# Performance work log

Measured on AMD Instinct MI355X. Metric: run time of the kernel, lower is better.

The kernel has to match this reference:

```python
import math
import jax, jax.numpy as jnp
import numpy as np

DIM = 512
STYLE_DIM = 512
WS = 8
RES = 64
HEADS = 16
SHIFT = WS // 2
B = 8
EPS = 1e-5


def _rel_pos_index(ws):
    # Faithful replica of the (non-standard) index construction in the source.
    coords = np.stack(np.meshgrid(np.arange(ws), np.arange(ws), indexing='ij')).reshape(2, -1)
    rc = (coords[:, :, None] - coords[:, None, :]).transpose(1, 2, 0).astype(np.int64)
    rc[:, :, 0] += ws - 1
    rc[:, :, 1] += ws - 1
    rc[:, :, 0] += 2 * ws - 1
    return jnp.asarray(rc.sum(-1))  # (ws*ws, ws*ws)


def _attn_mask2(res, ws):
    shift = ws // 2
    m = np.zeros((res, res), dtype=np.float32)
    cnt = 0
    for hs in [slice(0, -ws), slice(-ws, -shift), slice(-shift, None)]:
        for wsl in [slice(0, -ws), slice(-ws, -shift), slice(-shift, None)]:
            m[hs, wsl] = cnt
            cnt += 1
    mw = m.reshape(res // ws, ws, res // ws, ws).transpose(0, 2, 1, 3).reshape(-1, ws * ws)
    am = mw[:, None, :] - mw[:, :, None]  # (nW, N, N)
    return jnp.asarray(np.where(am != 0, -100.0, 0.0).astype(np.float32))


_RPI = _rel_pos_index(WS)
_MASK2 = _attn_mask2(RES, WS)


def _win_part(x, ws):
    Bc, H, W, C = x.shape
    x = x.reshape(Bc, H // ws, ws, W // ws, ws, C).transpose(0, 1, 3, 2, 4, 5)
    return x.reshape(-1, ws * ws, C)


def _win_rev(x, ws, H, W):
    nH, nW = H // ws, W // ws
    C = x.shape[-1]
    x = x.reshape(-1, nH, nW, ws, ws, C).transpose(0, 1, 3, 2, 4, 5)
    return x.reshape(-1, H, W, C)


def _adain(x, style, w, b):
    # x: (B, N, C); InstanceNorm1d over the token dim N per channel (biased var, no affine).
    scale = 1.0 / math.sqrt(w.shape[1])
    s = style @ (w * scale).T + b  # (B, 2C)
    C = x.shape[-1]
    gamma, beta = s[:, :C], s[:, C:]
    mean = x.mean(axis=1, keepdims=True)
    var = x.var(axis=1, keepdims=True)
    xn = (x - mean) / jnp.sqrt(var + EPS)
    return gamma[:, None, :] * xn + beta[:, None, :]


def _window_attn(q, k, v, ws, heads, rpb, rpi, mask):
    # q/k/v: (B, H, W, C)
    C = q.shape[-1]
    hd = C // heads
    qk_scale = hd ** -0.5
    qw = _win_part(q, ws)  # (Bw, N, C)
    kw = _win_part(k, ws)
    vw = _win_part(v, ws)
    Bw, N, _ = qw.shape
    qw = qw.reshape(Bw, N, heads, hd).transpose(0, 2, 1, 3)
    kw = kw.reshape(Bw, N, heads, hd).transpose(0, 2, 1, 3)
    vw = vw.reshape(Bw, N, heads, hd).transpose(0, 2, 1, 3)
    attn = jnp.einsum('bhnd,bhmd->bhnm', qw, kw) * qk_scale
    bias = rpb[rpi.reshape(-1)].reshape(N, N, heads).transpose(2, 0, 1)  # (h, N, N)
    attn = attn + bias[None]
    if mask is not None:
        nW = mask.shape[0]
        attn = attn.reshape(Bw // nW, nW, heads, N, N) + mask[None, :, None]
        attn = attn.reshape(Bw, heads, N, N)
    attn = jax.nn.softmax(attn, axis=-1)
    out = jnp.einsum('bhnm,bhmd->bhnd', attn, vw)
    return out.transpose(0, 2, 1, 3).reshape(Bw, N, C)


def _forward(x, style, ada1_w, ada1_b, qkv_w, qkv_b, rpb1, rpb2,
             proj_w, proj_b, ada2_w, ada2_b, mlp_w1, mlp_b1, mlp_w2, mlp_b2):
    H = W = RES
    Bc, N, C = x.shape
    shortcut = x
    xn = _adain(x, style, ada1_w, ada1_b)
    qkv = xn @ qkv_w.T + qkv_b  # (B, N, 3C)
    qkv = qkv.reshape(Bc, N, 3, C).transpose(2, 0, 1, 3).reshape(3, Bc, H, W, C)
    qkv1 = qkv[..., : C // 2]
    qkv2 = qkv[..., C // 2:]
    qkv2 = jnp.roll(qkv2, shift=(-SHIFT, -SHIFT), axis=(2, 3))
    x1 = _window_attn(qkv1[0], qkv1[1], qkv1[2], WS, HEADS // 2, rpb1, _RPI, None)
    x2 = _window_attn(qkv2[0], qkv2[1], qkv2[2], WS, HEADS // 2, rpb2, _RPI, _MASK2)
    x1 = _win_rev(x1, WS, H, W)
    x2 = _win_rev(x2, WS, H, W)
    x2 = jnp.roll(x2, shift=(SHIFT, SHIFT), axis=(1, 2))
    out = jnp.concatenate([x1, x2], axis=-1).reshape(Bc, N, C)
    out = out @ proj_w.T + proj_b
    out = shortcut + out
    xn2 = _adain(out, style, ada2_w, ada2_b)
    h = xn2 @ mlp_w1.T + mlp_b1
    h = jax.nn.gelu(h, approximate=False)  # erf-based gelu matches source
    h = h @ mlp_w2.T + mlp_b2
    return out + h


def setup_inputs() -> dict:
    key = jax.random.key(0)
    ks = jax.random.split(key, 16)
    rn = lambda k, shp, s: jax.random.normal(k, shp, dtype=jnp.float32) * s
    return {
        'x': rn(ks[0], (B, RES * RES, DIM), 1.0),
        'style': rn(ks[1], (B, STYLE_DIM), 1.0),
        'ada1_w': rn(ks[2], (2 * DIM, STYLE_DIM), 1.0),
        'ada1_b': rn(ks[3], (2 * DIM,), 0.02),
        'qkv_w': rn(ks[4], (3 * DIM, DIM), 0.02),
        'qkv_b': rn(ks[5], (3 * DIM,), 0.02),
        'rpb1': rn(ks[6], ((2 * WS - 1) ** 2, HEADS // 2), 0.02),
        'rpb2': rn(ks[7], ((2 * WS - 1) ** 2, HEADS // 2), 0.02),
        'proj_w': rn(ks[8], (DIM, DIM), 0.02),
        'proj_b': rn(ks[9], (DIM,), 0.02),
        'ada2_w': rn(ks[10], (2 * DIM, STYLE_DIM), 1.0),
        'ada2_b': rn(ks[11], (2 * DIM,), 0.02),
        'mlp_w1': rn(ks[12], (4 * DIM, DIM), 0.02),
        'mlp_b1': rn(ks[13], (4 * DIM,), 0.02),
        'mlp_w2': rn(ks[14], (DIM, 4 * DIM), 0.02),
        'mlp_b2': rn(ks[15], (DIM,), 0.02),
    }


def reference(x, style, ada1_w, ada1_b, qkv_w, qkv_b, rpb1, rpb2,
              proj_w, proj_b, ada2_w, ada2_b, mlp_w1, mlp_b1, mlp_w2, mlp_b2):
    return _forward(x, style, ada1_w, ada1_b, qkv_w, qkv_b, rpb1, rpb2,
                    proj_w, proj_b, ada2_w, ada2_b, mlp_w1, mlp_b1, mlp_w2, mlp_b2)
```

## Files before the change

kernel.cpp:

```cpp
#include <hip/hip_runtime.h>
#include <math.h>

typedef __attribute__((ext_vector_type(8))) short short8;
typedef __attribute__((ext_vector_type(4))) float f32x4;
typedef unsigned short ushort_t;
typedef unsigned long long ull_t;

__device__ __forceinline__ float bf2f(ushort_t u) {
    return __uint_as_float(((unsigned int)u) << 16);
}
__device__ __forceinline__ ushort_t f2bf(float f) {
    unsigned int u = __float_as_uint(f);
    unsigned int r = u + 0x7fffu + ((u >> 16) & 1u);
    return (ushort_t)(r >> 16);
}
__device__ __forceinline__ unsigned cvt_pk_bf16(float lo, float hi) {
    unsigned r;
    asm volatile("v_cvt_pk_bf16_f32 %0, %1, %2" : "=v"(r) : "v"(lo), "v"(hi));
    return r;
}

__device__ __forceinline__ void async_cp16(const void* g, void* l) {
    __builtin_amdgcn_global_load_lds((const __attribute__((address_space(1))) void*)g,
                                     (__attribute__((address_space(3))) void*)l, 16, 0, 0);
}

__device__ __forceinline__ float fast_gelu(float v) {
    float u2 = 2.0f * v * (0.7978845608028654f + 0.0356774081f * v * v);
    float e = __expf(u2);
    float r = 1.0f / (e + 1.0f);
    return v - v * r;
}

__global__ __launch_bounds__(256) void conv_zero(
        const float* __restrict__ qkv_w, ushort_t* __restrict__ qkv_wb,
        const float* __restrict__ proj_w, ushort_t* __restrict__ proj_wb,
        const float* __restrict__ w1, ushort_t* __restrict__ w1b,
        const float* __restrict__ w2, ushort_t* __restrict__ w2b,
        float* __restrict__ psum2, float* __restrict__ psq2,
        const float* __restrict__ rpb1, const float* __restrict__ rpb2,
        float* __restrict__ tbl0, float* __restrict__ tbl1) {
    int i = blockIdx.x * 256 + threadIdx.x;
    if (i < 786432) {
        qkv_wb[i] = f2bf(qkv_w[i]);
    } else if (i < 1048576) {
        int j = i - 786432; proj_wb[j] = f2bf(proj_w[j]);
    } else if (i < 2097152) {
        int j = i - 1048576; w1b[j] = f2bf(w1[j]);
    } else if (i < 3145728) {
        int j = i - 2097152; w2b[j] = f2bf(w2[j]);
    } else if (i < 3153920) {
        int j = i - 3145728;
        psum2[j] = 0.f; psq2[j] = 0.f;
    } else {
        int t = i - 3153920;
        if (t < 32768) {
            int h = t >> 12, ij = t & 4095;
            int qi = ij >> 6, kj = ij & 63;
            int idx = ((qi >> 3) - (kj >> 3)) + ((qi & 7) - (kj & 7)) + 29;
            tbl0[t] = rpb1[idx * 8 + h];
        } else {
            int u = t - 32768;
            int ij = u & 4095;
            int cls = (u >> 12) & 3;
            int h = u >> 14;
            int qi = ij >> 6, kj = ij & 63;
            int idx = ((qi >> 3) - (kj >> 3)) + ((qi & 7) - (kj & 7)) + 29;
            float v = rpb2[idx * 8 + h];
            int gh_i = (cls & 2) ? (((qi >> 3) < 4) ? 1 : 2) : 0;
            int gw_i = (cls & 1) ? (((qi & 7) < 4) ? 1 : 2) : 0;
            int gh_j = (cls & 2) ? (((kj >> 3) < 4) ? 1 : 2) : 0;
            int gw_j = (cls & 1) ? (((kj & 7) < 4) ? 1 : 2) : 0;
            if (gh_i * 3 + gw_i != gh_j * 3 + gw_j) v -= 100.f;
            tbl1[u] = v;
        }
    }
}

__global__ __launch_bounds__(256) void style_kernel(const float* __restrict__ style,
        const float* __restrict__ w1, const float* __restrict__ b1,
        const float* __restrict__ w2, const float* __restrict__ b2,
        float* __restrict__ s1, float* __restrict__ s2) {
    int t = blockIdx.x * 256 + threadIdx.x;
    int which = t >> 13;
    int idx = t & 8191;
    int b = idx >> 10, j = idx & 1023;
    const float* w = which ? w2 : w1;
    const float* bb = which ? b2 : b1;
    const float* st = style + b * 512;
    const float* wr = w + (size_t)j * 512;
    float acc = 0.f;
    for (int k = 0; k < 512; ++k) acc += st[k] * wr[k];
    float v = acc * 0.04419417382415922f + bb[j];
    (which ? s2 : s1)[idx] = v;
}

__global__ __launch_bounds__(512) void stats_part(const float* __restrict__ x,
        float* __restrict__ psum, float* __restrict__ psq) {
    int b = blockIdx.x >> 5;
    int ch = blockIdx.x & 31;
    int c = threadIdx.x;
    const float* p = x + ((size_t)b * 4096 + (size_t)ch * 128) * 512 + c;
    float s = 0.f, q = 0.f;
    for (int t = 0; t < 128; ++t) {
        float v = p[(size_t)t * 512];
        s += v; q += v * v;
    }
    psum[(size_t)blockIdx.x * 512 + c] = s;
    psq [(size_t)blockIdx.x * 512 + c] = q;
}

__global__ __launch_bounds__(256) void stats_fin(const float* __restrict__ psum,
        const float* __restrict__ psq, float* __restrict__ mean, float* __restrict__ rstd) {
    int i = blockIdx.x * 256 + threadIdx.x;
    int b = i >> 9, c = i & 511;
    float s = 0.f, q = 0.f;
    for (int ch = 0; ch < 32; ++ch) {
        s += psum[(size_t)(b * 32 + ch) * 512 + c];
        q += psq [(size_t)(b * 32 + ch) * 512 + c];
    }
    float m = s * (1.f / 4096.f);
    float v = q * (1.f / 4096.f) - m * m;
    mean[i] = m;
    rstd[i] = rsqrtf(v + 1e-5f);
}

__global__ __launch_bounds__(256) void stats_fin2(const float* __restrict__ psum2,
        const float* __restrict__ psq2, float* __restrict__ mean, float* __restrict__ rstd) {
    int i = blockIdx.x * 256 + threadIdx.x;
    float m = psum2[i] * (1.f / 4096.f);
    float v = psq2[i] * (1.f / 4096.f) - m * m;
    mean[i] = m;
    rstd[i] = rsqrtf(v + 1e-5f);
}

__global__ __launch_bounds__(256) void adain_kernel(const float* __restrict__ x,
        const float* __restrict__ s, const float* __restrict__ mean,
        const float* __restrict__ rstd, ushort_t* __restrict__ xn) {
    size_t i4 = (size_t)blockIdx.x * 256 + threadIdx.x;
    size_t e = i4 * 4;
    int b = (int)(e >> 21);
    int c = (int)(e & 511);
    float4 xv = *(const float4*)(x + e);
    float vals[4] = {xv.x, xv.y, xv.z, xv.w};
    ushort_t o[4];
#pragma unroll
    for (int j = 0; j < 4; ++j) {
        int cc = c + j;
        float g  = s[b * 1024 + cc];
        float be = s[b * 1024 + 512 + cc];
        float mn = mean[b * 512 + cc];
        float rs = rstd[b * 512 + cc];
        o[j] = f2bf(g * (vals[j] - mn) * rs + be);
    }
    ull_t packed = (ull_t)o[0] |
        ((ull_t)o[1] << 16) | ((ull_t)o[2] << 32) | ((ull_t)o[3] << 48);
    *(ull_t*)(xn + e) = packed;
}

template<int EPI>
__global__ __launch_bounds__(512, 2) void gemm256(
        const ushort_t* __restrict__ A, const ushort_t* __restrict__ Bw,
        const float* __restrict__ bias, const float* __restrict__ resid,
        float* __restrict__ outf, ushort_t* __restrict__ outh,
        float* __restrict__ psum2, float* __restrict__ psq2,
        int N, int K, int gridN, int ntiles, int lnt) {
    __shared__ ushort_t lds[65536];
    const int tid  = threadIdx.x;
    const int lane = tid & 63;
    const int wave = tid >> 6;
    const int wm = wave >> 2, wn = wave & 3;
    const int lm = lane & 15;
    const int kg = lane >> 4;
    const int nt = 1 << lnt;
    const int tpb = ntiles >> 8;

    const int orig = blockIdx.x;
    const int wgid = (orig & 7) * 32 + (orig >> 3);

    unsigned int lo0 = lm * 128 + ((kg * 16) ^ ((lm & 7) << 4));
    unsigned int lo1 = lo0 ^ 64;
    unsigned int vA0 = wm * 16384 + lo0;
    unsigned int vA1 = wm * 16384 + lo1;
    unsigned int vB0 = 65536 + (wn >> 1) * 16384 + (wn & 1) * 8192 + lo0;
    unsigned int vB1 = 65536 + (wn >> 1) * 16384 + (wn & 1) * 8192 + lo1;
    const char* ldsc = (const char*)lds;

    int off[2][2];
#pragma unroll
    for (int rnd = 0; rnd < 2; ++rnd) {
        int chunk = tid + rnd * 512;
        int row = chunk >> 3;
        int g = chunk & 7;
        int gsw = g ^ (row & 7);
#pragma unroll
        for (int h = 0; h < 2; ++h)
            off[h][rnd] = (h * 128 + row) * K + gsw * 8;
    }

    f32x4 acc[8][4];
#pragma unroll
    for (int m = 0; m < 8; ++m)
#pragma unroll
        for (int n = 0; n < 4; ++n)
#pragma unroll
            for (int r = 0; r < 4; ++r) acc[m][n][r] = 0.f;

    auto stage = [&](const ushort_t* __restrict__ mat, long bcur, long bnxt,
                     int dslot, int h, int tt, int isB) {
        long mb = (tt < nt) ? bcur : bnxt;
        int kt = tt & (nt - 1);
        const ushort_t* base = mat + mb + (kt << 6);
        ushort_t* dst = (ushort_t*)lds + isB * 32768 + dslot * 16384 + h * 8192 + tid * 8;
#pragma unroll
        for (int rnd = 0; rnd < 2; ++rnd)
            async_cp16(base + off[h][rnd], dst + rnd * 4096);
    };

    int tcur = wgid;
    int bm = tcur / gridN, bn = tcur - bm * gridN;
    long Am = (long)bm * 256 * K;
    long Bn = (long)bn * 256 * K;

    stage(A,  Am, Am, 0, 0, 0, 0); stage(A,  Am, Am, 0, 1, 0, 0);
    stage(Bw, Bn, Bn, 0, 0, 0, 1); stage(Bw, Bn, Bn, 0, 1, 0, 1);
    stage(Bw, Bn, Bn, 1, 0, 1, 1); stage(Bw, Bn, Bn, 1, 1, 1, 1);
    asm volatile("s_waitcnt vmcnt(4)" ::: "memory");
    __builtin_amdgcn_sched_barrier(0);
    __builtin_amdgcn_s_barrier();
    asm volatile("" ::: "memory");

    for (int ti = 0; ti < tpb; ++ti) {
        int tnxt = (ti + 1 < tpb) ? tcur + 256 : tcur;
        int bm2 = tnxt / gridN, bn2 = tnxt - bm2 * gridN;
        long Am2 = (long)bm2 * 256 * K;
        long Bn2 = (long)bn2 * 256 * K;

#pragma unroll 2
        for (int t = 0; t < nt; ++t) {
            const int c = t & 1;
            short8 bfr[4][2];
#pragma unroll
            for (int q = 0; q < 4; ++q) {
                short8 af[2][2];
#pragma unroll
                for (int mq = 0; mq < 2; ++mq) {
                    af[mq][0] = *(const short8*)(ldsc + vA0 + (q * 4096 + mq * 2048));
                    af[mq][1] = *(const short8*)(ldsc + vA1 + (q * 4096 + mq * 2048));
                }
                if (q == 0) {
#pragma unroll
                    for (int n = 0; n < 4; ++n) {
                        bfr[n][0] = *(const short8*)(ldsc + vB0 + n * 2048);
                        bfr[n][1] = *(const short8*)(ldsc + vB1 + n * 2048);
                    }
                }
                if      (q == 0) stage(A,  Am, Am2, c ^ 1, 0, t + 1, 0);
                else if (q == 1) stage(A,  Am, Am2, c ^ 1, 1, t + 1, 0);
                else if (q == 2) stage(Bw, Bn, Bn2, c,     0, t + 2, 1);
                else             stage(Bw, Bn, Bn2, c,     1, t + 2, 1);

                __builtin_amdgcn_s_setprio(1);
#pragma unroll
                for (int mq = 0; mq < 2; ++mq)
#pragma unroll
                    for (int n = 0; n < 4; ++n)
#pragma unroll
                        for (int ks = 0; ks < 2; ++ks)
                            acc[q * 2 + mq][n] = __builtin_amdgcn_mfma_f32_16x16x32_bf16(
                                af[mq][ks], bfr[n][ks], acc[q * 2 + mq][n], 0, 0, 0);
                __builtin_amdgcn_s_setprio(0);
                if (q == 3) {
                    asm volatile("s_waitcnt vmcnt(4)" ::: "memory");
                    __builtin_amdgcn_sched_barrier(0);
                }
                __builtin_amdgcn_s_barrier();
                asm volatile("" ::: "memory");
            }
            vA0 ^= 32768u; vA1 ^= 32768u; vB0 ^= 32768u; vB1 ^= 32768u;
        }

        const long tile_m = (long)bm * 256;
        const long tile_n = (long)bn * 256;
        float csum[4], csq[4];
        if (EPI == 1) {
#pragma unroll
            for (int n = 0; n < 4; ++n) { csum[n] = 0.f; csq[n] = 0.f; }
        }
#pragma unroll
        for (int m = 0; m < 8; ++m) {
            long row0 = tile_m + wm * 128 + m * 16 + kg * 4;
#pragma unroll
            for (int n = 0; n < 4; ++n) {
                long col = tile_n + wn * 64 + n * 16 + lm;
                float bb = bias[col];
#pragma unroll
                for (int r = 0; r < 4; ++r) {
                    long o = (row0 + r) * (long)N + col;
                    float v = acc[m][n][r] + bb;
                    if (EPI == 0) {
                        outh[o] = f2bf(v);
                    } else if (EPI == 1) {
                        float w = v + resid[o];
                        outf[o] = w;
                        csum[n] += w; csq[n] += w * w;
                    } else if (EPI == 2) {
                        outh[o] = f2bf(fast_gelu(v));
                    } else {
                        outf[o] += v;
                    }
                    acc[m][n][r] = 0.f;
                }
            }
        }
        if (EPI == 1) {
            int b = (int)(tile_m >> 12);
#pragma unroll
            for (int n = 0; n < 4; ++n) {
                int col = (int)(tile_n + wn * 64 + n * 16 + lm);
                atomicAdd(&psum2[b * 512 + col], csum[n]);
                atomicAdd(&psq2 [b * 512 + col], csq[n]);
            }
        }

        tcur = tnxt; bm = bm2; bn = bn2; Am = Am2; Bn = Bn2;
    }
}

__global__ __launch_bounds__(256) void attn_mfma(const ushort_t* __restrict__ qkv,
        const float* __restrict__ tbl0, const float* __restrict__ tbl1,
        ushort_t* __restrict__ attno) {
    __shared__ ushort_t lds[27648];
    const int tid = threadIdx.x;
    const int lane = tid & 63;
    const int wave = tid >> 6;
    const int job = blockIdx.x * 4 + wave;
    const int branch = job >> 12;
    const int w_idx  = (job >> 3) & 511;
    const int head   = job & 7;
    const int b = w_idx >> 6, win = w_idx & 63;
    const int wh = win >> 3, ww = win & 7;
    const int c0 = branch * 256 + head * 32;
    const int i_lo = lane & 15;
    const int kg = lane >> 4;

    ushort_t* Vt = lds + wave * 6912;
    ushort_t* P  = lds + wave * 6912 + 2304;

    auto tokof = [&](int p) {
        int hh = wh * 8 + (p >> 3), wp = ww * 8 + (p & 7);
        if (branch) { hh = (hh + 4) & 63; wp = (wp + 4) & 63; }
        return b * 4096 + hh * 64 + wp;
    };

    {
        const ushort_t* vp = qkv + (size_t)tokof(lane) * 1536 + 1024 + c0;
        short8 v0 = *(const short8*)(vp);
        short8 v1 = *(const short8*)(vp + 8);
        short8 v2 = *(const short8*)(vp + 16);
        short8 v3 = *(const short8*)(vp + 24);
#pragma unroll
        for (int e = 0; e < 8; ++e) {
            Vt[(e     ) * 72 + lane] = (ushort_t)v0[e];
            Vt[(e +  8) * 72 + lane] = (ushort_t)v1[e];
            Vt[(e + 16) * 72 + lane] = (ushort_t)v2[e];
            Vt[(e + 24) * 72 + lane] = (ushort_t)v3[e];
        }
    }

    short8 kf[4], qf[4];
#pragma unroll
    for (int m = 0; m < 4; ++m) {
        size_t rowb = (size_t)tokof(m * 16 + i_lo) * 1536;
        kf[m] = *(const short8*)(qkv + rowb + 512 + c0 + kg * 8);
        qf[m] = *(const short8*)(qkv + rowb + c0 + kg * 8);
    }

    f32x4 s[4][4];
#pragma unroll
    for (int mj = 0; mj < 4; ++mj)
#pragma unroll
        for (int ni = 0; ni < 4; ++ni)
#pragma unroll
            for (int r = 0; r < 4; ++r) s[mj][ni][r] = 0.f;
#pragma unroll
    for (int mj = 0; mj < 4; ++mj)
#pragma unroll
        for (int ni = 0; ni < 4; ++ni)
            s[mj][ni] = __builtin_amdgcn_mfma_f32_16x16x32_bf16(kf[mj], qf[ni], s[mj][ni], 0, 0, 0);

    const float* tb;
    if (branch == 0) {
        tb = tbl0 + head * 4096;
    } else {
        int cls = ((wh == 7) ? 2 : 0) | ((ww == 7) ? 1 : 0);
        tb = tbl1 + (head * 4 + cls) * 4096;
    }
#pragma unroll
    for (int ni = 0; ni < 4; ++ni) {
        int i = ni * 16 + i_lo;
#pragma unroll
        for (int mj = 0; mj < 4; ++mj) {
            float4 bv = *(const float4*)(tb + i * 64 + mj * 16 + kg * 4);
            s[mj][ni][0] = s[mj][ni][0] * 0.17677669529663687f + bv.x;
            s[mj][ni][1] = s[mj][ni][1] * 0.17677669529663687f + bv.y;
            s[mj][ni][2] = s[mj][ni][2] * 0.17677669529663687f + bv.z;
            s[mj][ni][3] = s[mj][ni][3] * 0.17677669529663687f + bv.w;
        }
    }

    float mx[4], rs[4];
#pragma unroll
    for (int ni = 0; ni < 4; ++ni) {
        float m = -1e30f;
#pragma unroll
        for (int mj = 0; mj < 4; ++mj)
#pragma unroll
            for (int r = 0; r < 4; ++r) m = fmaxf(m, s[mj][ni][r]);
        m = fmaxf(m, __shfl_xor(m, 16));
        m = fmaxf(m, __shfl_xor(m, 32));
        mx[ni] = m;
    }
#pragma unroll
    for (int ni = 0; ni < 4; ++ni) {
        float sum = 0.f;
#pragma unroll
        for (int mj = 0; mj < 4; ++mj)
#pragma unroll
            for (int r = 0; r < 4; ++r) {
                float e = __expf(s[mj][ni][r] - mx[ni]);
                s[mj][ni][r] = e;
                sum += e;
            }
        sum += __shfl_xor(sum, 16);
        sum += __shfl_xor(sum, 32);
        rs[ni] = sum;
    }

#pragma unroll
    for (int ni = 0; ni < 4; ++ni) {
        int i = ni * 16 + i_lo;
#pragma unroll
        for (int mj = 0; mj < 4; ++mj) {
            unsigned w0 = cvt_pk_bf16(s[mj][ni][0], s[mj][ni][1]);
            unsigned w1 = cvt_pk_bf16(s[mj][ni][2], s[mj][ni][3]);
            ull_t w = (ull_t)w0 | ((ull_t)w1 << 32);
            *(ull_t*)&P[i * 72 + mj * 16 + kg * 4] = w;
        }
    }
    asm volatile("s_waitcnt lgkmcnt(0)" ::: "memory");
    __builtin_amdgcn_sched_barrier(0);

    short8 va[2][2];
    short8 pb[4][2];
#pragma unroll
    for (int md = 0; md < 2; ++md)
#pragma unroll
        for (int ks = 0; ks < 2; ++ks)
            va[md][ks] = *(const short8*)&Vt[(md * 16 + i_lo) * 72 + ks * 32 + kg * 8];
#pragma unroll
    for (int ni = 0; ni < 4; ++ni)
#pragma unroll
        for (int ks = 0; ks < 2; ++ks)
            pb[ni][ks] = *(const short8*)&P[(ni * 16 + i_lo) * 72 + ks * 32 + kg * 8];

    f32x4 o[2][4];
#pragma unroll
    for (int md = 0; md < 2; ++md)
#pragma unroll
        for (int ni = 0; ni < 4; ++ni)
#pragma unroll
            for (int r = 0; r < 4; ++r) o[md][ni][r] = 0.f;
#pragma unroll
    for (int md = 0; md < 2; ++md)
#pragma unroll
        for (int ni = 0; ni < 4; ++ni)
#pragma unroll
            for (int ks = 0; ks < 2; ++ks)
                o[md][ni] = __builtin_amdgcn_mfma_f32_16x16x32_bf16(va[md][ks], pb[ni][ks], o[md][ni], 0, 0, 0);

#pragma unroll
    for (int ni = 0; ni < 4; ++ni) {
        float inv = 1.f / rs[ni];
        ushort_t* op = attno + (size_t)tokof(ni * 16 + i_lo) * 512 + c0;
#pragma unroll
        for (int md = 0; md < 2; ++md) {
            ushort_t h0 = f2bf(o[md][ni][0] * inv);
            ushort_t h1 = f2bf(o[md][ni][1] * inv);
            ushort_t h2 = f2bf(o[md][ni][2] * inv);
            ushort_t h3 = f2bf(o[md][ni][3] * inv);
            ull_t w = (ull_t)h0 | ((ull_t)h1 << 16) | ((ull_t)h2 << 32) | ((ull_t)h3 << 48);
            *(ull_t*)(op + md * 16 + kg * 4) = w;
        }
    }
}

extern "C" void kernel_launch(void* const* d_in, const int* in_sizes, int n_in,
                              void* d_out, int out_size, void* d_ws, size_t ws_size,
                              hipStream_t stream) {
    const float* x      = (const float*)d_in[0];
    const float* style  = (const float*)d_in[1];
    const float* ada1_w = (const float*)d_in[2];
    const float* ada1_b = (const float*)d_in[3];
    const float* qkv_w  = (const float*)d_in[4];
    const float* qkv_b  = (const float*)d_in[5];
    const float* rpb1   = (const float*)d_in[6];
    const float* rpb2   = (const float*)d_in[7];
    const float* proj_w = (const float*)d_in[8];
    const float* proj_b = (const float*)d_in[9];
    const float* ada2_w = (const float*)d_in[10];
    const float* ada2_b = (const float*)d_in[11];
    const float* mlp_w1 = (const float*)d_in[12];
    const float* mlp_b1 = (const float*)d_in[13];
    const float* mlp_w2 = (const float*)d_in[14];
    const float* mlp_b2 = (const float*)d_in[15];
    float* outf = (float*)d_out;

    char* W = (char*)d_ws;
    ushort_t* qkvb    = (ushort_t*)(W);
    ushort_t* attno   = (ushort_t*)(W + 100663296);
    ushort_t* hbuf    = (ushort_t*)(W);
    ushort_t* xn      = (ushort_t*)(W + 134217728);
    ushort_t* qkv_wb  = (ushort_t*)(W + 167772160);
    ushort_t* proj_wb = (ushort_t*)(W + 167772160 + 1572864);
    ushort_t* w1b     = (ushort_t*)(W + 167772160 + 2097152);
    ushort_t* w2b     = (ushort_t*)(W + 167772160 + 4194304);
    float* freg  = (float*)(W + 167772160 + 6291456);
    float* s1    = freg;
    float* s2    = freg + 8192;
    float* mean1 = freg + 16384;
    float* rstd1 = freg + 20480;
    float* mean2 = freg + 24576;
    float* rstd2 = freg + 28672;
    float* psum  = freg + 32768;
    float* psq   = freg + 163840;
    float* psum2 = freg + 294912;
    float* psq2  = freg + 303104;
    float* tbl0  = freg + 311296;
    float* tbl1  = freg + 344064;

    conv_zero<<<12960, 256, 0, stream>>>(qkv_w, qkv_wb, proj_w, proj_wb,
                                         mlp_w1, w1b, mlp_w2, w2b, psum2, psq2,
                                         rpb1, rpb2, tbl0, tbl1);

    style_kernel<<<64, 256, 0, stream>>>(style, ada1_w, ada1_b, ada2_w, ada2_b, s1, s2);

    stats_part<<<256, 512, 0, stream>>>(x, psum, psq);
    stats_fin<<<16, 256, 0, stream>>>(psum, psq, mean1, rstd1);
    adain_kernel<<<16384, 256, 0, stream>>>(x, s1, mean1, rstd1, xn);

    gemm256<0><<<256, 512, 0, stream>>>(xn, qkv_wb, qkv_b, nullptr, nullptr, qkvb,
                                        nullptr, nullptr, 1536, 512, 6, 768, 3);

    attn_mfma<<<2048, 256, 0, stream>>>(qkvb, tbl0, tbl1, attno);

    gemm256<1><<<256, 512, 0, stream>>>(attno, proj_wb, proj_b, x, outf, nullptr,
                                        psum2, psq2, 512, 512, 2, 256, 3);

    stats_fin2<<<16, 256, 0, stream>>>(psum2, psq2, mean2, rstd2);
    adain_kernel<<<16384, 256, 0, stream>>>(outf, s2, mean2, rstd2, xn);

    gemm256<2><<<256, 512, 0, stream>>>(xn, w1b, mlp_b1, nullptr, nullptr, hbuf,
                                        nullptr, nullptr, 2048, 512, 8, 1024, 3);
    gemm256<3><<<256, 512, 0, stream>>>(hbuf, w2b, mlp_b2, nullptr, outf, nullptr,
                                        nullptr, nullptr, 512, 2048, 2, 256, 5);
}
```

Baseline: 423.1 us.

## Split style dot products, widen AdaIN vectors, simplify GEMM B prefetch

Result: slower. 435.8 us (+3.0%).

```diff
diff --git a/kernel.cpp b/kernel.cpp
--- a/kernel.cpp
+++ b/kernel.cpp
@@ -82,17 +82,27 @@
         const float* __restrict__ w2, const float* __restrict__ b2,
         float* __restrict__ s1, float* __restrict__ s2) {
     int t = blockIdx.x * 256 + threadIdx.x;
-    int which = t >> 13;
-    int idx = t & 8191;
+    int oi = t >> 2;
+    int kc = t & 3;
+    int which = oi >> 13;
+    int idx = oi & 8191;
     int b = idx >> 10, j = idx & 1023;
     const float* w = which ? w2 : w1;
     const float* bb = which ? b2 : b1;
-    const float* st = style + b * 512;
-    const float* wr = w + (size_t)j * 512;
+    const float4* st = (const float4*)(style + b * 512 + kc * 128);
+    const float4* wr = (const float4*)(w + (size_t)j * 512 + kc * 128);
     float acc = 0.f;
-    for (int k = 0; k < 512; ++k) acc += st[k] * wr[k];
-    float v = acc * 0.04419417382415922f + bb[j];
-    (which ? s2 : s1)[idx] = v;
+#pragma unroll
+    for (int k = 0; k < 32; ++k) {
+        float4 a = st[k], c = wr[k];
+        acc += a.x * c.x + a.y * c.y + a.z * c.z + a.w * c.w;
+    }
+    acc += __shfl_xor(acc, 1);
+    acc += __shfl_xor(acc, 2);
+    if (kc == 0) {
+        float v = acc * 0.04419417382415922f + bb[j];
+        (which ? s2 : s1)[idx] = v;
+    }
 }
 
 __global__ __launch_bounds__(512) void stats_part(const float* __restrict__ x,
@@ -137,25 +147,24 @@
 __global__ __launch_bounds__(256) void adain_kernel(const float* __restrict__ x,
         const float* __restrict__ s, const float* __restrict__ mean,
         const float* __restrict__ rstd, ushort_t* __restrict__ xn) {
-    size_t i4 = (size_t)blockIdx.x * 256 + threadIdx.x;
-    size_t e = i4 * 4;
+    size_t i8 = (size_t)blockIdx.x * 256 + threadIdx.x;
+    size_t e = i8 * 8;
     int b = (int)(e >> 21);
     int c = (int)(e & 511);
-    float4 xv = *(const float4*)(x + e);
-    float vals[4] = {xv.x, xv.y, xv.z, xv.w};
-    ushort_t o[4];
-#pragma unroll
-    for (int j = 0; j < 4; ++j) {
+    float4 x0 = *(const float4*)(x + e);
+    float4 x1 = *(const float4*)(x + e + 4);
+    float vals[8] = {x0.x, x0.y, x0.z, x0.w, x1.x, x1.y, x1.z, x1.w};
+    short8 o;
+#pragma unroll
+    for (int j = 0; j < 8; ++j) {
         int cc = c + j;
         float g  = s[b * 1024 + cc];
         float be = s[b * 1024 + 512 + cc];
         float mn = mean[b * 512 + cc];
         float rs = rstd[b * 512 + cc];
-        o[j] = f2bf(g * (vals[j] - mn) * rs + be);
-    }
-    ull_t packed = (ull_t)o[0] |
-        ((ull_t)o[1] << 16) | ((ull_t)o[2] << 32) | ((ull_t)o[3] << 48);
-    *(ull_t*)(xn + e) = packed;
+        o[j] = (short)f2bf(g * (vals[j] - mn) * rs + be);
+    }
+    *(short8*)(xn + e) = o;
 }
 
 template<int EPI>
@@ -224,8 +233,7 @@
 
     stage(A,  Am, Am, 0, 0, 0, 0); stage(A,  Am, Am, 0, 1, 0, 0);
     stage(Bw, Bn, Bn, 0, 0, 0, 1); stage(Bw, Bn, Bn, 0, 1, 0, 1);
-    stage(Bw, Bn, Bn, 1, 0, 1, 1); stage(Bw, Bn, Bn, 1, 1, 1, 1);
-    asm volatile("s_waitcnt vmcnt(4)" ::: "memory");
+    asm volatile("s_waitcnt vmcnt(0)" ::: "memory");
     __builtin_amdgcn_sched_barrier(0);
     __builtin_amdgcn_s_barrier();
     asm volatile("" ::: "memory");
@@ -257,8 +265,8 @@
                 }
                 if      (q == 0) stage(A,  Am, Am2, c ^ 1, 0, t + 1, 0);
                 else if (q == 1) stage(A,  Am, Am2, c ^ 1, 1, t + 1, 0);
-                else if (q == 2) stage(Bw, Bn, Bn2, c,     0, t + 2, 1);
-                else             stage(Bw, Bn, Bn2, c,     1, t + 2, 1);
+                else if (q == 2) stage(Bw, Bn, Bn2, c ^ 1, 0, t + 1, 1);
+                else             stage(Bw, Bn, Bn2, c ^ 1, 1, t + 1, 1);
 
                 __builtin_amdgcn_s_setprio(1);
 #pragma unroll
@@ -271,11 +279,11 @@
                                 af[mq][ks], bfr[n][ks], acc[q * 2 + mq][n], 0, 0, 0);
                 __builtin_amdgcn_s_setprio(0);
                 if (q == 3) {
-                    asm volatile("s_waitcnt vmcnt(4)" ::: "memory");
+                    asm volatile("s_waitcnt vmcnt(0)" ::: "memory");
                     __builtin_amdgcn_sched_barrier(0);
+                    __builtin_amdgcn_s_barrier();
+                    asm volatile("" ::: "memory");
                 }
-                __builtin_amdgcn_s_barrier();
-                asm volatile("" ::: "memory");
             }
             vA0 ^= 32768u; vA1 ^= 32768u; vB0 ^= 32768u; vB1 ^= 32768u;
         }
@@ -543,11 +551,11 @@
                                          mlp_w1, w1b, mlp_w2, w2b, psum2, psq2,
                                          rpb1, rpb2, tbl0, tbl1);
 
-    style_kernel<<<64, 256, 0, stream>>>(style, ada1_w, ada1_b, ada2_w, ada2_b, s1, s2);
+    style_kernel<<<256, 256, 0, stream>>>(style, ada1_w, ada1_b, ada2_w, ada2_b, s1, s2);
 
     stats_part<<<256, 512, 0, stream>>>(x, psum, psq);
     stats_fin<<<16, 256, 0, stream>>>(psum, psq, mean1, rstd1);
-    adain_kernel<<<16384, 256, 0, stream>>>(x, s1, mean1, rstd1, xn);
+    adain_kernel<<<8192, 256, 0, stream>>>(x, s1, mean1, rstd1, xn);
 
     gemm256<0><<<256, 512, 0, stream>>>(xn, qkv_wb, qkv_b, nullptr, nullptr, qkvb,
                                         nullptr, nullptr, 1536, 512, 6, 768, 3);
@@ -558,7 +566,7 @@
                                         psum2, psq2, 512, 512, 2, 256, 3);
 
     stats_fin2<<<16, 256, 0, stream>>>(psum2, psq2, mean2, rstd2);
-    adain_kernel<<<16384, 256, 0, stream>>>(outf, s2, mean2, rstd2, xn);
+    adain_kernel<<<8192, 256, 0, stream>>>(outf, s2, mean2, rstd2, xn);
 
     gemm256<2><<<256, 512, 0, stream>>>(xn, w1b, mlp_b1, nullptr, nullptr, hbuf,
                                         nullptr, nullptr, 2048, 512, 8, 1024, 3);
```
